# Kernel tuning notes

Measured on AMD Instinct MI355X. Metric: run time of the kernel, lower is better.

The kernel has to match this reference:

```python
import jax, jax.numpy as jnp
import numpy as np

N = 100000          # num_nodes
E = 1250000         # num_edges
H = 64              # node_hidden_size
T = 2               # num_rounds


def setup_inputs() -> dict:
    key = jax.random.key(0)
    ks = jax.random.split(key, 10)
    s = 0.1  # init scale for weights
    return {
        "x": jax.random.normal(ks[0], (N, H), dtype=jnp.float32),
        "edge_index": jax.random.randint(ks[1], (2, E), 0, N, dtype=jnp.int64),
        "edge_attr": jax.random.normal(ks[2], (E, 1), dtype=jnp.float32),
        # message layers: Linear(2H+1 -> H), one per round
        "msg_W": jax.random.normal(ks[3], (T, H, 2 * H + 1), dtype=jnp.float32) * s,
        "msg_b": jax.random.normal(ks[4], (T, H), dtype=jnp.float32) * s,
        # GRUCell params, gate order (r, z, n) as in torch
        "gru_Wih": jax.random.normal(ks[5], (T, 3 * H, H), dtype=jnp.float32) * s,
        "gru_bih": jax.random.normal(ks[6], (T, 3 * H), dtype=jnp.float32) * s,
        "gru_Whh": jax.random.normal(ks[7], (T, 3 * H, H), dtype=jnp.float32) * s,
        "gru_bhh": jax.random.normal(ks[8], (T, 3 * H), dtype=jnp.float32) * s,
    }


def _gru_cell(inp, h, Wih, bih, Whh, bhh):
    # torch.nn.GRUCell math, gate order r, z, n
    gi = inp @ Wih.T + bih   # [N, 3H]
    gh = h @ Whh.T + bhh     # [N, 3H]
    i_r, i_z, i_n = jnp.split(gi, 3, axis=1)
    h_r, h_z, h_n = jnp.split(gh, 3, axis=1)
    r = jax.nn.sigmoid(i_r + h_r)
    z = jax.nn.sigmoid(i_z + h_z)
    n = jnp.tanh(i_n + r * h_n)
    return (1.0 - z) * n + z * h


def reference(x, edge_index, edge_attr, msg_W, msg_b, gru_Wih, gru_bih, gru_Whh, gru_bhh):
    row, col = edge_index[0], edge_index[1]
    num_rounds = msg_W.shape[0]
    for t in range(num_rounds):
        src = x[row]    # [E, H]
        dest = x[col]   # [E, H]
        m_input = jnp.concatenate([dest, src, edge_attr], axis=1)  # [E, 2H+1]
        messages = m_input @ msg_W[t].T + msg_b[t]                 # [E, H]
        agg = jax.ops.segment_sum(messages, row, num_segments=x.shape[0])  # [N, H]
        x = _gru_cell(agg, x, gru_Wih[t], gru_bih[t], gru_Whh[t], gru_bhh[t])
    return x
```

## Files before the change

kernel.cpp:

```cpp
#include <hip/hip_runtime.h>
#include <hip/hip_bf16.h>
#include <hip/hip_fp16.h>

#define H 64
#define CAP 48

typedef __attribute__((ext_vector_type(8))) short short8;
typedef __attribute__((ext_vector_type(4))) float float4v;

__device__ __forceinline__ short f2bf_bits(float f) {
    union { __hip_bfloat16 b; short s; } u;
    u.b = __float2bfloat16(f);
    return u.s;
}
__device__ __forceinline__ float bf2f(unsigned short s) {
    union { unsigned int u; float f; } v;
    v.u = ((unsigned int)s) << 16;
    return v.f;
}
__device__ __forceinline__ void split8(const float* p, short8& hi, short8& lo) {
    float4v f0 = *(const float4v*)p;
    float4v f1 = *(const float4v*)(p + 4);
#pragma unroll
    for (int j = 0; j < 8; j++) {
        float f = (j < 4) ? f0[j] : f1[j - 4];
        short h = f2bf_bits(f);
        float fh = bf2f((unsigned short)h);
        hi[j] = h;
        lo[j] = f2bf_bits(f - fh);
    }
}
__device__ __forceinline__ void zero8(short8& hi, short8& lo) {
#pragma unroll
    for (int j = 0; j < 8; j++) { hi[j] = 0; lo[j] = 0; }
}

#define MFMA(a, b, c) __builtin_amdgcn_mfma_f32_16x16x32_bf16(a, b, c, 0, 0, 0)

__global__ __launch_bounds__(256) void count_prep(
    const int* __restrict__ row, int* __restrict__ deg, int* __restrict__ lpos,
    int E, int EB,
    const float* __restrict__ msg_W,
    const float* __restrict__ Wih, const float* __restrict__ Whh,
    short* __restrict__ msgfrag, short* __restrict__ grufrag, int T)
{
    if ((int)blockIdx.x < EB) {
        int e = blockIdx.x * 256 + threadIdx.x;
        if (e < E) lpos[e] = atomicAdd(&deg[row[e]], 1);
        return;
    }
    const int lane = threadIdx.x & 63;
    int unit = (blockIdx.x - EB) * 4 + (threadIdx.x >> 6);
    const int kq = (lane >> 4) * 8;
    if (unit < T * 16) {
        const int slot = unit & 15, t = unit >> 4;
        const int tile = slot >> 1, ks = slot & 1;
        const float* W = msg_W + (size_t)t * H * 129;
        const int wrow = (tile & 3) * 16 + (lane & 15);
        const int coff = (tile < 4) ? 0 : 64;
        short8 hi, lo;
        split8(W + (size_t)wrow * 129 + coff + ks * 32 + kq, hi, lo);
        short8* out = (short8*)(msgfrag + (size_t)t * 16384);
        out[slot * 64 + lane] = hi;
        out[16 * 64 + slot * 64 + lane] = lo;
    } else {
        unit -= T * 16;
        if (unit >= T * 48) return;
        const int slot = unit % 48, t = unit / 48;
        const int tile = slot >> 1, ks = slot & 1;
        const float* Wp = (tile < 12)
            ? (Wih + (size_t)t * 192 * H + ((size_t)(tile * 16 + (lane & 15))) * H)
            : (Whh + (size_t)t * 192 * H + ((size_t)((tile - 12) * 16 + (lane & 15))) * H);
        short8 hi, lo;
        split8(Wp + ks * 32 + kq, hi, lo);
        short8* out = (short8*)(grufrag + (size_t)t * 49152);
        out[slot * 64 + lane] = hi;
        out[48 * 64 + slot * 64 + lane] = lo;
    }
}

__global__ __launch_bounds__(256) void scatter_cast(
    const int* __restrict__ row, const int* __restrict__ col,
    const float* __restrict__ attr, const int* __restrict__ lpos,
    int2* __restrict__ edata, int E, int EB,
    const float* __restrict__ x_in, __half* __restrict__ xh, int NH8)
{
    if ((int)blockIdx.x < EB) {
        int e = blockIdx.x * 256 + threadIdx.x;
        if (e < E) {
            int p = lpos[e];
            if (p < CAP) {
                int2 v;
                v.x = col[e];
                v.y = __float_as_int(attr[e]);
                edata[(size_t)row[e] * CAP + p] = v;
            }
        }
    } else {
        int i = (blockIdx.x - EB) * 256 + threadIdx.x;
        if (i < NH8) {
            const float* p = x_in + (size_t)i * 8;
            float4v f0 = *(const float4v*)p;
            float4v f1 = *(const float4v*)(p + 4);
            short8 hv;
#pragma unroll
            for (int u = 0; u < 8; u++) {
                float f = (u < 4) ? f0[u] : f1[u - 4];
                hv[u] = __half_as_short(__float2half(f));
            }
            *(short8*)(xh + (size_t)i * 8) = hv;
        }
    }
}

__global__ __launch_bounds__(64) void aggregate(
    const int* __restrict__ deg, const int2* __restrict__ edata,
    const __half* __restrict__ xh,
    short* __restrict__ s_hi, short* __restrict__ s_lo,
    float2* __restrict__ asum2, int N)
{
    const int lane = threadIdx.x & 63;
    const int g = lane >> 3, cl = lane & 7;
    const int n = blockIdx.x * 8 + g;
    int cnt = 0;
    if (n < N) { cnt = deg[n]; if (cnt > CAP) cnt = CAP; }
    const int2* ebase = edata + (size_t)n * CAP;
    float acc[8] = {0.f,0.f,0.f,0.f,0.f,0.f,0.f,0.f};
    float aacc = 0.f;
    for (int j = 0; j < cnt; j += 8) {
        int2 e[8];
#pragma unroll
        for (int u = 0; u < 8; u++) {
            int idx = j + u; if (idx > cnt - 1) idx = cnt - 1;
            e[u] = ebase[idx];
        }
        short8 h[8];
#pragma unroll
        for (int u = 0; u < 8; u++) {
            int c = e[u].x;
            c = (c < 0) ? 0 : (c >= N ? N - 1 : c);
            h[u] = *(const short8*)(xh + (size_t)c * H + cl * 8);
        }
#pragma unroll
        for (int u = 0; u < 8; u++) {
            const bool val = (j + u < cnt);
            const float w = val ? 1.f : 0.f;
            aacc += val ? __int_as_float(e[u].y) : 0.f;
#pragma unroll
            for (int k = 0; k < 8; k++)
                acc[k] = fmaf(w, __half2float(__ushort_as_half((unsigned short)h[u][k])), acc[k]);
        }
    }
    if (n < N) {
        short8 hi8, lo8;
#pragma unroll
        for (int u = 0; u < 8; u++) {
            float v = acc[u];
            short hbits = f2bf_bits(v);
            hi8[u] = hbits;
            lo8[u] = f2bf_bits(v - bf2f((unsigned short)hbits));
        }
        *(short8*)(s_hi + (size_t)n * H + cl * 8) = hi8;
        *(short8*)(s_lo + (size_t)n * H + cl * 8) = lo8;
        if (cl == 0) asum2[n] = make_float2(aacc, (float)cnt);
    }
}

#define SLD 68
__global__ __launch_bounds__(64) void fused_msg_gru(
    const short* __restrict__ s_hi, const short* __restrict__ s_lo,
    const float2* __restrict__ asum2,
    const float* xf,
    float* x, __half* __restrict__ xh,
    const short* __restrict__ mfrag, const short* __restrict__ gfrag,
    const float* __restrict__ Wt, const float* __restrict__ mb,
    const float* __restrict__ bih, const float* __restrict__ bhh,
    int N, int write_xh)
{
    __shared__ float scratch[2][16 * SLD];
    const int lane = threadIdx.x & 63;
    const int base = blockIdx.x * 32;
    if (base >= N) return;
    const int arow = lane & 15;
    const int kq = (lane >> 4) * 8;
    const int colb = lane & 15;
    const int rq4 = (lane >> 4) * 4;
    const short8* mhi = (const short8*)mfrag;
    const short8* mlo = mhi + 16 * 64;
    const short8* ghi = (const short8*)gfrag;
    const short8* glo = ghi + 48 * 64;

    short8 sfh[2][2], sfl[2][2], xfh[2][2], xfl[2][2];
    bool mv[2];
    int m_a[2];
#pragma unroll
    for (int rt = 0; rt < 2; rt++) {
        m_a[rt] = base + rt * 16 + arow;
        mv[rt] = (m_a[rt] < N);
#pragma unroll
        for (int ks = 0; ks < 2; ks++) {
            if (mv[rt]) {
                sfh[rt][ks] = *(const short8*)(s_hi + (size_t)m_a[rt] * H + ks * 32 + kq);
                sfl[rt][ks] = *(const short8*)(s_lo + (size_t)m_a[rt] * H + ks * 32 + kq);
                split8(xf + (size_t)m_a[rt] * H + ks * 32 + kq, xfh[rt][ks], xfl[rt][ks]);
            } else { zero8(sfh[rt][ks], sfl[rt][ks]); zero8(xfh[rt][ks], xfl[rt][ks]); }
        }
    }
    float2 da[2][4];
#pragma unroll
    for (int rt = 0; rt < 2; rt++)
#pragma unroll
        for (int r = 0; r < 4; r++) {
            const int m = base + rt * 16 + rq4 + r;
            da[rt][r] = (m < N) ? asum2[m] : make_float2(0.f, 0.f);
        }

#pragma unroll
    for (int ct = 0; ct < 4; ct++) {
        float4v accd[2], accs[2];
#pragma unroll
        for (int rt = 0; rt < 2; rt++) {
            accd[rt] = (float4v){0.f, 0.f, 0.f, 0.f};
            accs[rt] = (float4v){0.f, 0.f, 0.f, 0.f};
        }
#pragma unroll
        for (int ks = 0; ks < 2; ks++) {
            short8 bh = mhi[(ct * 2 + ks) * 64 + lane];
            short8 bl = mlo[(ct * 2 + ks) * 64 + lane];
            short8 ch = mhi[((4 + ct) * 2 + ks) * 64 + lane];
            short8 cl8 = mlo[((4 + ct) * 2 + ks) * 64 + lane];
#pragma unroll
            for (int rt = 0; rt < 2; rt++) {
                accd[rt] = MFMA(sfh[rt][ks], bh, accd[rt]);
                accd[rt] = MFMA(sfl[rt][ks], bh, accd[rt]);
                accd[rt] = MFMA(sfh[rt][ks], bl, accd[rt]);
                accs[rt] = MFMA(xfh[rt][ks], ch, accs[rt]);
                accs[rt] = MFMA(xfl[rt][ks], ch, accs[rt]);
                accs[rt] = MFMA(xfh[rt][ks], cl8, accs[rt]);
            }
        }
        const int j = ct * 16 + colb;
        const float bj = mb[j];
        const float wa = Wt[(size_t)j * 129 + 128];
#pragma unroll
        for (int rt = 0; rt < 2; rt++)
#pragma unroll
            for (int r = 0; r < 4; r++) {
                float v = accd[rt][r] + da[rt][r].y * (accs[rt][r] + bj)
                        + da[rt][r].x * wa;
                scratch[rt][(rq4 + r) * SLD + j] = v;
            }
    }
    asm volatile("s_waitcnt lgkmcnt(0)" ::: "memory");
    short8 agh[2][2], agl[2][2];
#pragma unroll
    for (int rt = 0; rt < 2; rt++)
#pragma unroll
        for (int ks = 0; ks < 2; ks++)
            split8(scratch[rt] + arow * SLD + ks * 32 + kq, agh[rt][ks], agl[rt][ks]);

#pragma unroll
    for (int ct = 0; ct < 4; ct++) {
        float4v ai[2][3], ao[2][3];
#pragma unroll
        for (int rt = 0; rt < 2; rt++)
#pragma unroll
            for (int g2 = 0; g2 < 3; g2++) {
                ai[rt][g2] = (float4v){0.f, 0.f, 0.f, 0.f};
                ao[rt][g2] = (float4v){0.f, 0.f, 0.f, 0.f};
            }
#pragma unroll
        for (int ks = 0; ks < 2; ks++) {
#pragma unroll
            for (int g2 = 0; g2 < 3; g2++) {
                short8 bh = ghi[((g2 * 4 + ct) * 2 + ks) * 64 + lane];
                short8 bl = glo[((g2 * 4 + ct) * 2 + ks) * 64 + lane];
                short8 hh = ghi[((12 + g2 * 4 + ct) * 2 + ks) * 64 + lane];
                short8 hl = glo[((12 + g2 * 4 + ct) * 2 + ks) * 64 + lane];
#pragma unroll
                for (int rt = 0; rt < 2; rt++) {
                    ai[rt][g2] = MFMA(agh[rt][ks], bh, ai[rt][g2]);
                    ai[rt][g2] = MFMA(agl[rt][ks], bh, ai[rt][g2]);
                    ai[rt][g2] = MFMA(agh[rt][ks], bl, ai[rt][g2]);
                    ao[rt][g2] = MFMA(xfh[rt][ks], hh, ao[rt][g2]);
                    ao[rt][g2] = MFMA(xfl[rt][ks], hh, ao[rt][g2]);
                    ao[rt][g2] = MFMA(xfh[rt][ks], hl, ao[rt][g2]);
                }
            }
        }
        const int j = ct * 16 + colb;
        const float b_ir = bih[j], b_iz = bih[64 + j], b_in = bih[128 + j];
        const float b_hr = bhh[j], b_hz = bhh[64 + j], b_hn = bhh[128 + j];
#pragma unroll
        for (int rt = 0; rt < 2; rt++)
#pragma unroll
            for (int r = 0; r < 4; r++) {
                const int m = base + rt * 16 + rq4 + r;
                float ir = ai[rt][0][r] + b_ir;
                float iz = ai[rt][1][r] + b_iz;
                float in_ = ai[rt][2][r] + b_in;
                float hr = ao[rt][0][r] + b_hr;
                float hz = ao[rt][1][r] + b_hz;
                float hn = ao[rt][2][r] + b_hn;
                float rr = 1.f / (1.f + __expf(-(ir + hr)));
                float zz = 1.f / (1.f + __expf(-(iz + hz)));
                float e2 = __expf(2.f * (in_ + rr * hn));
                float nn = 1.f - 2.f / (e2 + 1.f);
                float hold = (m < N) ? xf[(size_t)m * H + j] : 0.f;
                scratch[rt][(rq4 + r) * SLD + j] = (1.f - zz) * nn + zz * hold;
            }
    }
    asm volatile("s_waitcnt lgkmcnt(0)" ::: "memory");

#pragma unroll
    for (int rt = 0; rt < 2; rt++) {
        if (!mv[rt]) continue;
        float4v o[4];
#pragma unroll
        for (int q4 = 0; q4 < 4; q4++)
            o[q4] = *(const float4v*)(scratch[rt] + arow * SLD + (lane >> 4) * 16 + q4 * 4);
        float4v* xp = (float4v*)(x + (size_t)m_a[rt] * H + (lane >> 4) * 16);
        xp[0] = o[0]; xp[1] = o[1]; xp[2] = o[2]; xp[3] = o[3];
        if (write_xh) {
            short8 hv0, hv1;
#pragma unroll
            for (int u = 0; u < 8; u++) {
                hv0[u] = __half_as_short(__float2half(o[u >> 2][u & 3]));
                hv1[u] = __half_as_short(__float2half(o[2 + (u >> 2)][u & 3]));
            }
            *(short8*)(xh + (size_t)m_a[rt] * H + (lane >> 4) * 16) = hv0;
            *(short8*)(xh + (size_t)m_a[rt] * H + (lane >> 4) * 16 + 8) = hv1;
        }
    }
}

extern "C" void kernel_launch(void* const* d_in, const int* in_sizes, int n_in,
                              void* d_out, int out_size, void* d_ws, size_t ws_size,
                              hipStream_t stream) {
    const float* x_in  = (const float*)d_in[0];
    const int*   ei    = (const int*)d_in[1];
    const float* attr  = (const float*)d_in[2];
    const float* msg_W = (const float*)d_in[3];
    const float* msg_b = (const float*)d_in[4];
    const float* Wih   = (const float*)d_in[5];
    const float* bih   = (const float*)d_in[6];
    const float* Whh   = (const float*)d_in[7];
    const float* bhh   = (const float*)d_in[8];

    const int N = in_sizes[0] / H;
    const int E = in_sizes[2];
    const int T = in_sizes[4] / H;
    const int* row = ei;
    const int* col = ei + E;

    float*  x       = (float*)d_out;
    short*  s_hi    = (short*)d_ws;
    short*  s_lo    = s_hi + (size_t)N * H;
    int*    lpos    = (int*)s_lo;
    __half* xh      = (__half*)(s_lo + (size_t)N * H);
    float2* asum2   = (float2*)(xh + (size_t)N * H);
    int*    deg     = (int*)(asum2 + N);
    int2*   edata   = (int2*)(deg + N);
    short*  msgfrag = (short*)(edata + (size_t)N * CAP);
    short*  grufrag = msgfrag + (size_t)T * 16384;

    const int eb  = (E + 255) / 256;
    const int nh8 = (N * H) / 8;
    const int cb  = (nh8 + 255) / 256;
    const int pb  = (T * 16 + T * 48 + 3) / 4;

    hipMemsetAsync(deg, 0, (size_t)N * sizeof(int), stream);

    count_prep<<<eb + pb, 256, 0, stream>>>(
        row, deg, lpos, E, eb, msg_W, Wih, Whh, msgfrag, grufrag, T);
    scatter_cast<<<eb + cb, 256, 0, stream>>>(
        row, col, attr, lpos, edata, E, eb, x_in, xh, nh8);

    const int agg_blocks = (N + 7) / 8;
    const int fus_blocks = (N + 31) / 32;

    for (int t = 0; t < T; t++) {
        aggregate<<<agg_blocks, 64, 0, stream>>>(
            deg, edata, xh, s_hi, s_lo, asum2, N);
        fused_msg_gru<<<fus_blocks, 64, 0, stream>>>(
            s_hi, s_lo, asum2,
            (t == 0) ? x_in : x, x, xh,
            msgfrag + (size_t)t * 16384, grufrag + (size_t)t * 49152,
            msg_W + (size_t)t * H * (2 * H + 1), msg_b + (size_t)t * H,
            bih + (size_t)t * 3 * H, bhh + (size_t)t * 3 * H,
            N, (t + 1 < T) ? 1 : 0);
    }
}
```

Measured before the change: 323.2 us.

## Fuse neighbor aggregation into message+GRU kernel with ping-pong fp16 buffers

Merges the separate aggregate kernel into the fused message/GRU kernel: each 32-node block first gathers neighbor fp16 features into LDS scratch, then splits them into bf16 hi/lo for the MFMA path. This removes the global round trip of s_hi/s_lo/asum2 and one launch per round. The fp16 node copy is double-buffered so reads of the previous round's features don't race with the writes. The trade-off is that the irregular gather now runs inside the register- and LDS-heavy GRU kernel, which may reduce occupancy and limit latency hiding.

```diff
diff --git a/kernel.cpp b/kernel.cpp
--- a/kernel.cpp
+++ b/kernel.cpp
@@ -113,71 +113,19 @@
     }
 }
 
-__global__ __launch_bounds__(64) void aggregate(
+#define SLD 68
+__global__ __launch_bounds__(64) void agg_msg_gru(
     const int* __restrict__ deg, const int2* __restrict__ edata,
-    const __half* __restrict__ xh,
-    short* __restrict__ s_hi, short* __restrict__ s_lo,
-    float2* __restrict__ asum2, int N)
-{
-    const int lane = threadIdx.x & 63;
-    const int g = lane >> 3, cl = lane & 7;
-    const int n = blockIdx.x * 8 + g;
-    int cnt = 0;
-    if (n < N) { cnt = deg[n]; if (cnt > CAP) cnt = CAP; }
-    const int2* ebase = edata + (size_t)n * CAP;
-    float acc[8] = {0.f,0.f,0.f,0.f,0.f,0.f,0.f,0.f};
-    float aacc = 0.f;
-    for (int j = 0; j < cnt; j += 8) {
-        int2 e[8];
-#pragma unroll
-        for (int u = 0; u < 8; u++) {
-            int idx = j + u; if (idx > cnt - 1) idx = cnt - 1;
-            e[u] = ebase[idx];
-        }
-        short8 h[8];
-#pragma unroll
-        for (int u = 0; u < 8; u++) {
-            int c = e[u].x;
-            c = (c < 0) ? 0 : (c >= N ? N - 1 : c);
-            h[u] = *(const short8*)(xh + (size_t)c * H + cl * 8);
-        }
-#pragma unroll
-        for (int u = 0; u < 8; u++) {
-            const bool val = (j + u < cnt);
-            const float w = val ? 1.f : 0.f;
-            aacc += val ? __int_as_float(e[u].y) : 0.f;
-#pragma unroll
-            for (int k = 0; k < 8; k++)
-                acc[k] = fmaf(w, __half2float(__ushort_as_half((unsigned short)h[u][k])), acc[k]);
-        }
-    }
-    if (n < N) {
-        short8 hi8, lo8;
-#pragma unroll
-        for (int u = 0; u < 8; u++) {
-            float v = acc[u];
-            short hbits = f2bf_bits(v);
-            hi8[u] = hbits;
-            lo8[u] = f2bf_bits(v - bf2f((unsigned short)hbits));
-        }
-        *(short8*)(s_hi + (size_t)n * H + cl * 8) = hi8;
-        *(short8*)(s_lo + (size_t)n * H + cl * 8) = lo8;
-        if (cl == 0) asum2[n] = make_float2(aacc, (float)cnt);
-    }
-}
-
-#define SLD 68
-__global__ __launch_bounds__(64) void fused_msg_gru(
-    const short* __restrict__ s_hi, const short* __restrict__ s_lo,
-    const float2* __restrict__ asum2,
+    const __half* __restrict__ xh_r,
     const float* xf,
-    float* x, __half* __restrict__ xh,
+    float* x, __half* __restrict__ xh_w,
     const short* __restrict__ mfrag, const short* __restrict__ gfrag,
     const float* __restrict__ Wt, const float* __restrict__ mb,
     const float* __restrict__ bih, const float* __restrict__ bhh,
     int N, int write_xh)
 {
     __shared__ float scratch[2][16 * SLD];
+    __shared__ float2 adeg[32];
     const int lane = threadIdx.x & 63;
     const int base = blockIdx.x * 32;
     if (base >= N) return;
@@ -185,11 +133,57 @@
     const int kq = (lane >> 4) * 8;
     const int colb = lane & 15;
     const int rq4 = (lane >> 4) * 4;
+    const int g = lane >> 3, cl = lane & 7;
     const short8* mhi = (const short8*)mfrag;
     const short8* mlo = mhi + 16 * 64;
     const short8* ghi = (const short8*)gfrag;
     const short8* glo = ghi + 48 * 64;
 
+#pragma unroll
+    for (int p = 0; p < 4; p++) {
+        const int n = base + p * 8 + g;
+        int cnt = 0;
+        if (n < N) { cnt = deg[n]; if (cnt > CAP) cnt = CAP; }
+        const int2* ebase = edata + (size_t)n * CAP;
+        float acc[8] = {0.f,0.f,0.f,0.f,0.f,0.f,0.f,0.f};
+        float aacc = 0.f;
+        for (int j = 0; j < cnt; j += 8) {
+            int2 e[8];
+#pragma unroll
+            for (int u = 0; u < 8; u++) {
+                int idx = j + u; if (idx > cnt - 1) idx = cnt - 1;
+                e[u] = ebase[idx];
+            }
+            short8 h[8];
+#pragma unroll
+            for (int u = 0; u < 8; u++) {
+                int c = e[u].x;
+                c = (c < 0) ? 0 : (c >= N ? N - 1 : c);
+                h[u] = *(const short8*)(xh_r + (size_t)c * H + cl * 8);
+            }
+#pragma unroll
+            for (int u = 0; u < 8; u++) {
+                const bool val = (j + u < cnt);
+                const float w = val ? 1.f : 0.f;
+                aacc += val ? __int_as_float(e[u].y) : 0.f;
+#pragma unroll
+                for (int k = 0; k < 8; k++)
+                    acc[k] = fmaf(w, __half2float(__ushort_as_half((unsigned short)h[u][k])), acc[k]);
+            }
+        }
+        float* sr = scratch[p >> 1] + ((p & 1) * 8 + g) * SLD + cl * 8;
+        *(float4v*)sr       = (float4v){acc[0], acc[1], acc[2], acc[3]};
+        *(float4v*)(sr + 4) = (float4v){acc[4], acc[5], acc[6], acc[7]};
+        if (cl == 0) adeg[p * 8 + g] = make_float2(aacc, (float)cnt);
+    }
+    asm volatile("s_waitcnt lgkmcnt(0)" ::: "memory");
+
+    float2 da[2][4];
+#pragma unroll
+    for (int rt = 0; rt < 2; rt++)
+#pragma unroll
+        for (int r = 0; r < 4; r++) da[rt][r] = adeg[rt * 16 + rq4 + r];
+
     short8 sfh[2][2], sfl[2][2], xfh[2][2], xfl[2][2];
     bool mv[2];
     int m_a[2];
@@ -199,21 +193,11 @@
         mv[rt] = (m_a[rt] < N);
 #pragma unroll
         for (int ks = 0; ks < 2; ks++) {
-            if (mv[rt]) {
-                sfh[rt][ks] = *(const short8*)(s_hi + (size_t)m_a[rt] * H + ks * 32 + kq);
-                sfl[rt][ks] = *(const short8*)(s_lo + (size_t)m_a[rt] * H + ks * 32 + kq);
-                split8(xf + (size_t)m_a[rt] * H + ks * 32 + kq, xfh[rt][ks], xfl[rt][ks]);
-            } else { zero8(sfh[rt][ks], sfl[rt][ks]); zero8(xfh[rt][ks], xfl[rt][ks]); }
-        }
-    }
-    float2 da[2][4];
-#pragma unroll
-    for (int rt = 0; rt < 2; rt++)
-#pragma unroll
-        for (int r = 0; r < 4; r++) {
-            const int m = base + rt * 16 + rq4 + r;
-            da[rt][r] = (m < N) ? asum2[m] : make_float2(0.f, 0.f);
-        }
+            split8(scratch[rt] + arow * SLD + ks * 32 + kq, sfh[rt][ks], sfl[rt][ks]);
+            if (mv[rt]) split8(xf + (size_t)m_a[rt] * H + ks * 32 + kq, xfh[rt][ks], xfl[rt][ks]);
+            else        zero8(xfh[rt][ks], xfl[rt][ks]);
+        }
+    }
 
 #pragma unroll
     for (int ct = 0; ct < 4; ct++) {
@@ -328,8 +312,8 @@
                 hv0[u] = __half_as_short(__float2half(o[u >> 2][u & 3]));
                 hv1[u] = __half_as_short(__float2half(o[2 + (u >> 2)][u & 3]));
             }
-            *(short8*)(xh + (size_t)m_a[rt] * H + (lane >> 4) * 16) = hv0;
-            *(short8*)(xh + (size_t)m_a[rt] * H + (lane >> 4) * 16 + 8) = hv1;
+            *(short8*)(xh_w + (size_t)m_a[rt] * H + (lane >> 4) * 16) = hv0;
+            *(short8*)(xh_w + (size_t)m_a[rt] * H + (lane >> 4) * 16 + 8) = hv1;
         }
     }
 }
@@ -354,12 +338,10 @@
     const int* col = ei + E;
 
     float*  x       = (float*)d_out;
-    short*  s_hi    = (short*)d_ws;
-    short*  s_lo    = s_hi + (size_t)N * H;
-    int*    lpos    = (int*)s_lo;
-    __half* xh      = (__half*)(s_lo + (size_t)N * H);
-    float2* asum2   = (float2*)(xh + (size_t)N * H);
-    int*    deg     = (int*)(asum2 + N);
+    __half* xh_a    = (__half*)d_ws;
+    __half* xh_b    = xh_a + (size_t)N * H;
+    int*    lpos    = (int*)(xh_b + (size_t)N * H);
+    int*    deg     = lpos + E;
     int2*   edata   = (int2*)(deg + N);
     short*  msgfrag = (short*)(edata + (size_t)N * CAP);
     short*  grufrag = msgfrag + (size_t)T * 16384;
@@ -374,17 +356,16 @@
     count_prep<<<eb + pb, 256, 0, stream>>>(
         row, deg, lpos, E, eb, msg_W, Wih, Whh, msgfrag, grufrag, T);
     scatter_cast<<<eb + cb, 256, 0, stream>>>(
-        row, col, attr, lpos, edata, E, eb, x_in, xh, nh8);
-
-    const int agg_blocks = (N + 7) / 8;
-    const int fus_blocks = (N + 31) / 32;
+        row, col, attr, lpos, edata, E, eb, x_in, xh_a, nh8);
+
+    const int mg_blocks = (N + 31) / 32;
 
     for (int t = 0; t < T; t++) {
-        aggregate<<<agg_blocks, 64, 0, stream>>>(
-            deg, edata, xh, s_hi, s_lo, asum2, N);
-        fused_msg_gru<<<fus_blocks, 64, 0, stream>>>(
-            s_hi, s_lo, asum2,
-            (t == 0) ? x_in : x, x, xh,
+        const __half* xh_r = (t & 1) ? xh_b : xh_a;
+        __half*       xh_w = (t & 1) ? xh_a : xh_b;
+        agg_msg_gru<<<mg_blocks, 64, 0, stream>>>(
+            deg, edata, xh_r,
+            (t == 0) ? x_in : x, x, xh_w,
             msgfrag + (size_t)t * 16384, grufrag + (size_t)t * 49152,
             msg_W + (size_t)t * H * (2 * H + 1), msg_b + (size_t)t * H,
             bih + (size_t)t * 3 * H, bhh + (size_t)t * 3 * H,
```

Measured after the change: 309.0 us. -4.4%, faster.
